# Kernel tuning notes

Hardware: AMD Instinct MI355X
Metric: run time of the kernel (lower is better)

The kernel has to match this reference:

```python
import jax, jax.numpy as jnp
import numpy as np

B, N, C = 2, 2048, 2048
H, KV = 16, 4          # query heads, kv heads
D = C // H             # head_dim = 128
ROPE_BASE = 10000.0


def rope_cos_sin(position_ids, dim):
    # interleaved RoPE: freqs for even indices, repeated pairwise to full dim
    inv_freq = 1.0 / (ROPE_BASE ** (jnp.arange(0, dim, 2, dtype=jnp.float32) / dim))
    ang = position_ids[..., None].astype(jnp.float32) * inv_freq   # [B, N, D/2]
    cos = jnp.repeat(jnp.cos(ang), 2, axis=-1)                     # [B, N, D]
    sin = jnp.repeat(jnp.sin(ang), 2, axis=-1)
    return cos, sin


def rotate_half_interleaved(x):
    # (x0, x1, x2, x3, ...) -> (-x1, x0, -x3, x2, ...)
    x1 = x[..., 0::2]
    x2 = x[..., 1::2]
    return jnp.stack([-x2, x1], axis=-1).reshape(x.shape)


def apply_rotary(x, cos, sin):
    # x: [B, h, N, D]; cos/sin: [B, N, D]
    return x * cos[:, None] + rotate_half_interleaved(x) * sin[:, None]


def setup_inputs() -> dict:
    key = jax.random.key(0)
    ks = jax.random.split(key, 5)
    s = 0.02
    return dict(
        x=jax.random.normal(ks[0], (B, N, C), jnp.float32),
        position_ids=jnp.tile(jnp.arange(N, dtype=jnp.int32), (B, 1)),
        Wq=jax.random.normal(ks[1], (C, C), jnp.float32) * s,
        bq=jnp.zeros((C,), jnp.float32),
        Wk=jax.random.normal(ks[2], (C, KV * D), jnp.float32) * s,
        bk=jnp.zeros((KV * D,), jnp.float32),
        Wv=jax.random.normal(ks[3], (C, KV * D), jnp.float32) * s,
        bv=jnp.zeros((KV * D,), jnp.float32),
        Wo=jax.random.normal(ks[4], (C, C), jnp.float32) * s,
    )


def reference(x, position_ids, Wq, bq, Wk, bk, Wv, bv, Wo):
    Bx, Nx, Cx = x.shape
    q = (x @ Wq + bq).reshape(Bx, Nx, H, D).transpose(0, 2, 1, 3)   # [B,H,N,D]
    k = (x @ Wk + bk).reshape(Bx, Nx, KV, D).transpose(0, 2, 1, 3)  # [B,KV,N,D]
    v = (x @ Wv + bv).reshape(Bx, Nx, KV, D).transpose(0, 2, 1, 3)

    cos, sin = rope_cos_sin(position_ids, D)
    q = apply_rotary(q, cos, sin)
    k = apply_rotary(k, cos, sin)

    # GQA expand: head h uses kv head h // groups (matches unsqueeze+expand+reshape)
    groups = H // KV
    k = jnp.repeat(k, groups, axis=1)   # [B,H,N,D]
    v = jnp.repeat(v, groups, axis=1)

    attn = jnp.einsum('bhqd,bhkd->bhqk', q, k) * (D ** -0.5)        # [B,H,N,N]
    causal_mask = jnp.triu(jnp.ones((Nx, Nx), dtype=bool), 1)
    attn = jnp.where(causal_mask, -jnp.inf, attn)
    attn = jax.nn.softmax(attn, axis=-1)

    out = jnp.einsum('bhqk,bhkd->bhqd', attn, v)
    out = out.transpose(0, 2, 1, 3).reshape(Bx, Nx, Cx)
    return out @ Wo
```

## Files before the change

kernel.cpp:

```cpp
#include <hip/hip_runtime.h>
#include <cstdint>
#include <type_traits>

typedef unsigned short u16;
typedef unsigned int u32;
typedef __bf16 bf16x8 __attribute__((ext_vector_type(8)));
typedef float f32x4 __attribute__((ext_vector_type(4)));

constexpr int BB = 2;
constexpr int SEQ = 2048;
constexpr int CH = 2048;
constexpr int NH = 16;
constexpr int NKV = 4;
constexpr int HD = 128;
constexpr int QKVC = CH + 2 * NKV * HD;

#define DI __device__ __forceinline__

DI u16 f2b(float x) {
  u32 u = __float_as_uint(x);
  u = u + 0x7FFFu + ((u >> 16) & 1u);
  return (u16)(u >> 16);
}
DI float b2f(u16 u) { return __uint_as_float(((u32)u) << 16); }

DI u32 pack2bf(float lo, float hi) {
  return __builtin_amdgcn_perm(__float_as_uint(hi), __float_as_uint(lo), 0x07060302u);
}

DI void glds16(const void* g, void* l) {
  __builtin_amdgcn_global_load_lds(
      (__attribute__((address_space(1))) void*)(uintptr_t)g,
      (__attribute__((address_space(3))) void*)(u32)(uintptr_t)l, 16, 0, 0);
}

__global__ __launch_bounds__(256) void xconv_kernel(const float* __restrict__ in,
                                                    u16* __restrict__ out, int n4) {
  int i = blockIdx.x * 256 + threadIdx.x;
  if (i < n4) {
    float4 v = *(const float4*)&in[(size_t)i * 4];
    ushort4 o;
    o.x = f2b(v.x); o.y = f2b(v.y); o.z = f2b(v.z); o.w = f2b(v.w);
    *(ushort4*)&out[(size_t)i * 4] = o;
  }
}

__global__ __launch_bounds__(256) void wtrans4_kernel(
    const float* __restrict__ Wq, const float* __restrict__ Wk,
    const float* __restrict__ Wv, const float* __restrict__ Wo,
    u16* __restrict__ wqkvt, u16* __restrict__ wot) {
  const int z = blockIdx.z;
  const float* in;
  u16* out;
  int Cc;
  if (z == 0)      { in = Wq; out = wqkvt;                                Cc = CH; }
  else if (z == 1) { in = Wk; out = wqkvt + (size_t)CH * CH;              Cc = NKV * HD; }
  else if (z == 2) { in = Wv; out = wqkvt + (size_t)(CH + NKV * HD) * CH; Cc = NKV * HD; }
  else             { in = Wo; out = wot;                                  Cc = CH; }
  if ((int)blockIdx.y * 64 >= Cc) return;

  __shared__ u16 tile[64 * 65];
  const int r0 = blockIdx.x * 64, c0 = blockIdx.y * 64;
  const int tid = threadIdx.x;
  for (int c = tid; c < 1024; c += 256) {
    int r = c >> 4, col = (c & 15) * 4;
    float4 v = *(const float4*)&in[(size_t)(r0 + r) * Cc + c0 + col];
    tile[r * 65 + col + 0] = f2b(v.x);
    tile[r * 65 + col + 1] = f2b(v.y);
    tile[r * 65 + col + 2] = f2b(v.z);
    tile[r * 65 + col + 3] = f2b(v.w);
  }
  __syncthreads();
  for (int c = tid; c < 1024; c += 256) {
    int r = c >> 4, col = (c & 15) * 4;
    ushort4 v;
    v.x = tile[(col + 0) * 65 + r];
    v.y = tile[(col + 1) * 65 + r];
    v.z = tile[(col + 2) * 65 + r];
    v.w = tile[(col + 3) * 65 + r];
    *(ushort4*)&out[(size_t)(c0 + r) * CH + r0 + col] = v;
  }
}

__global__ __launch_bounds__(256) void vtrans_kernel(const u16* __restrict__ in,
                                                     u16* __restrict__ out) {
  __shared__ u16 tile[64 * 65];
  const int s = blockIdx.z, n0 = blockIdx.x * 64, d0 = blockIdx.y * 64;
  const int tid = threadIdx.x;
  const u16* ip = in + (size_t)s * SEQ * HD + (size_t)n0 * HD + d0;
  u16* op = out + (size_t)s * HD * SEQ + (size_t)d0 * SEQ + n0;
  for (int c = tid; c < 1024; c += 256) {
    int r = c >> 4, col = (c & 15) * 4;
    ushort4 v = *(const ushort4*)&ip[(size_t)r * HD + col];
    tile[r * 65 + col + 0] = v.x;
    tile[r * 65 + col + 1] = v.y;
    tile[r * 65 + col + 2] = v.z;
    tile[r * 65 + col + 3] = v.w;
  }
  __syncthreads();
  for (int c = tid; c < 1024; c += 256) {
    int r = c >> 4, col = (c & 15) * 4;
    ushort4 v;
    v.x = tile[(col + 0) * 65 + r];
    v.y = tile[(col + 1) * 65 + r];
    v.z = tile[(col + 2) * 65 + r];
    v.w = tile[(col + 3) * 65 + r];
    int u = col;
    int w = (u & 3) | (((u >> 5) & 1) << 2) | (((u >> 2) & 3) << 3) | (((u >> 4) & 1) << 5);
    int glp = (w >> 3) ^ (r & 7);
    int colp = glp * 8 + (w & 7);
    *(ushort4*)&op[(size_t)r * SEQ + colp] = v;
  }
}

template <int MODE>
__global__ __launch_bounds__(512, 2) void gemm256_kernel(
    const u16* __restrict__ A, const u16* __restrict__ Bt,
    u16* __restrict__ Cb, float* __restrict__ Cf, u16* __restrict__ Vn,
    const float* __restrict__ bq, const float* __restrict__ bk,
    const float* __restrict__ bv, int M, int Nn, int K) {
  constexpr int BM = (MODE == 0) ? 256 : 128;
  constexpr int MI = BM / 32;
  constexpr int NPH = MI / 2;
  extern __shared__ char smem[];
  u16* As = (u16*)smem;
  u16* Bs = As + 2 * BM * 64;

  const int tid = threadIdx.x;
  const int lane = tid & 63, wave = tid >> 6;
  const int wrow = wave >> 2, wcol = wave & 3;
  const int lm = lane & 15, lq = lane >> 4;
  const int m0 = blockIdx.x * BM, n0 = blockIdx.y * 256;
  const int srow = tid >> 3;
  const int sswz = (tid & 7) ^ (srow & 7);

  f32x4 acc[MI][4] = {};

  auto stageA = [&](int kt, int b) {
#pragma unroll
    for (int s = 0; s < BM / 64; s++)
      glds16(A + (size_t)(m0 + s * 64 + srow) * K + kt + sswz * 8,
             (char*)As + b * (BM * 128) + (s * 64 + wave * 8) * 128);
  };
  auto stageB = [&](int kt, int b) {
#pragma unroll
    for (int s = 0; s < 4; s++)
      glds16(Bt + (size_t)(n0 + s * 64 + srow) * K + kt + sswz * 8,
             (char*)Bs + b * (256 * 128) + (s * 64 + wave * 8) * 128);
  };

  const int NT = K >> 6;
  stageA(0, 0);
  stageB(0, 0);
  asm volatile("s_waitcnt vmcnt(0)" ::: "memory");
  __builtin_amdgcn_s_barrier();

  for (int T = 0; T < NT; T++) {
    const int buf = T & 1;
    const u16* Asb = As + buf * (BM * 64);
    const u16* Bsb = Bs + buf * (256 * 64);
    const int kt1 = (T + 1) << 6;
    const bool pf = (T + 1 < NT);
    bf16x8 bfv[4][2];
#pragma unroll
    for (int q = 0; q < NPH; q++) {
      bf16x8 af[2][2];
#pragma unroll
      for (int ii = 0; ii < 2; ii++)
#pragma unroll
        for (int kk = 0; kk < 2; kk++)
          af[ii][kk] = *(const bf16x8*)&Asb[(wrow * (BM / 2) + (q * 2 + ii) * 16 + lm) * 64 +
                                            (((kk * 4 + lq) ^ (lm & 7)) * 8)];
      if (q == 0) {
#pragma unroll
        for (int j = 0; j < 4; j++)
#pragma unroll
          for (int kk = 0; kk < 2; kk++)
            bfv[j][kk] = *(const bf16x8*)&Bsb[(wcol * 64 + j * 16 + lm) * 64 +
                                              (((kk * 4 + lq) ^ (lm & 7)) * 8)];
        if (pf) {
          stageA(kt1, buf ^ 1);
          if (NPH == 2) stageB(kt1, buf ^ 1);
        }
      }
      if (NPH == 4 && q == 1 && pf) stageB(kt1, buf ^ 1);
      __builtin_amdgcn_s_barrier();
      asm volatile("s_waitcnt lgkmcnt(0)" ::: "memory");
      __builtin_amdgcn_sched_barrier(0);
      __builtin_amdgcn_s_setprio(1);
#pragma unroll
      for (int ii = 0; ii < 2; ii++)
#pragma unroll
        for (int j = 0; j < 4; j++)
#pragma unroll
          for (int kk = 0; kk < 2; kk++)
            acc[q * 2 + ii][j] = __builtin_amdgcn_mfma_f32_16x16x32_bf16(
                af[ii][kk], bfv[j][kk], acc[q * 2 + ii][j], 0, 0, 0);
      __builtin_amdgcn_s_setprio(0);
      if (q == NPH - 1) asm volatile("s_waitcnt vmcnt(0)" ::: "memory");
      __builtin_amdgcn_s_barrier();
    }
  }

#pragma unroll
  for (int i = 0; i < MI; i++) {
    const int mg = m0 + wrow * (BM / 2) + i * 16 + lq * 4;
#pragma unroll
    for (int j = 0; j < 4; j++) {
      const int ng = n0 + wcol * 64 + j * 16 + lm;
      float bias = 0.f;
      if (MODE == 0)
        bias = (ng < CH) ? bq[ng] : (ng < CH + NKV * HD ? bk[ng - CH] : bv[ng - CH - NKV * HD]);
#pragma unroll
      for (int r = 0; r < 4; r++) {
        float v = acc[i][j][r] + bias;
        if (MODE == 0) {
          if (ng >= CH + NKV * HD) {
            int tok = mg + r;
            int bidx = tok >> 11, n = tok & (SEQ - 1);
            int vcol = ng - (CH + NKV * HD);
            int kh = vcol >> 7, d = vcol & (HD - 1);
            Vn[((size_t)(bidx * NKV + kh) * SEQ + n) * HD + d] = f2b(v);
          } else {
            Cb[(size_t)(mg + r) * Nn + ng] = f2b(v);
          }
        } else {
          Cf[(size_t)(mg + r) * Nn + ng] = v;
        }
      }
    }
  }
}

__global__ __launch_bounds__(256) void rope_kernel(
    const u16* __restrict__ qkv, const int* __restrict__ pos,
    u16* __restrict__ Qo, u16* __restrict__ Ko) {
  __shared__ float cs_s[64], sn_s[64];
  const int tok = blockIdx.x;
  const int b = tok >> 11, n = tok & (SEQ - 1);
  const int t = threadIdx.x;
  const u16* row = qkv + (size_t)tok * QKVC;
  const float LN1E4_64 = 0.14391156831212788f;

  if (t < 64) {
    float ang = (float)pos[tok] * expf(-(float)t * LN1E4_64);
    float sn, cs;
    sincosf(ang, &sn, &cs);
    cs_s[t] = cs;
    sn_s[t] = sn;
  }
  __syncthreads();

  for (int idx = t; idx < NH * 64; idx += 256) {
    int hh = idx >> 6, i = idx & 63;
    float cs = cs_s[i], sn = sn_s[i];
    float q0v = b2f(row[hh * 128 + 2 * i]);
    float q1v = b2f(row[hh * 128 + 2 * i + 1]);
    size_t off = ((size_t)(b * NH + hh) * SEQ + n) * HD + 2 * i;
    Qo[off] = f2b(q0v * cs - q1v * sn);
    Qo[off + 1] = f2b(q1v * cs + q0v * sn);
  }
  {
    int kh = t >> 6, i = t & 63;
    float cs = cs_s[i], sn = sn_s[i];
    float k0v = b2f(row[CH + kh * 128 + 2 * i]);
    float k1v = b2f(row[CH + kh * 128 + 2 * i + 1]);
    int d0 = 2 * i;
    int g = d0 >> 3;
    int gp = (g & 8) | ((g ^ n) & 7);
    int dp = gp * 8 + (d0 & 7);
    size_t off = ((size_t)(b * NKV + kh) * SEQ + n) * HD + dp;
    Ko[off] = f2b(k0v * cs - k1v * sn);
    Ko[off + 1] = f2b(k1v * cs + k0v * sn);
  }
}

__global__ __launch_bounds__(256, 2) void flash_kernel(
    const u16* __restrict__ Q, const u16* __restrict__ Kk,
    const u16* __restrict__ Vt, u16* __restrict__ Oo) {
  __shared__ u16 Kb[2][64 * 128];
  __shared__ u16 Vb[2][144 * 64];
  const int tid = threadIdx.x, lane = tid & 63, wave = tid >> 6;
  const int lm = lane & 15, lq = lane >> 4;
  const int p = blockIdx.x;
  const int h = blockIdx.y, b = blockIdx.z;
  const int q0A = p * 64, q0B = (31 - p) * 64;
  const int kvh = h >> 2;
  const u16* Qg = Q + (size_t)(b * NH + h) * SEQ * HD;
  const u16* Kg = Kk + (size_t)(b * NKV + kvh) * SEQ * HD;
  const u16* Vg = Vt + (size_t)(b * NKV + kvh) * HD * SEQ;

  if (tid < 128) Vb[tid >> 6][128 * 64 + (tid & 63)] = 0x3F80;

  bf16x8 qf[2][4];
#pragma unroll
  for (int qg = 0; qg < 2; qg++) {
    const int q0g = qg ? q0B : q0A;
    const u16* qrow = Qg + (size_t)(q0g + wave * 16 + lm) * HD;
#pragma unroll
    for (int kd = 0; kd < 4; kd++)
      qf[qg][kd] = *(const bf16x8*)&qrow[kd * 32 + lq * 8];
  }

  f32x4 oacc[2][8] = {};
  f32x4 oaccS[2] = {};
  const float SCL2 = 0.12754325f;
  const int nIter = 32 - p;

  auto stage = [&](int kv0, int bufi) {
    const char* kb = (const char*)(Kg + (size_t)kv0 * HD);
    char* kl = (char*)&Kb[bufi][0];
    const char* vbb = (const char*)(Vg + (size_t)kv0);
    char* vl = (char*)&Vb[bufi][0];
#pragma unroll
    for (int c = 0; c < 4; c++) {
      int ch = wave * 4 + c;
      glds16(kb + ch * 1024 + lane * 16, kl + ch * 1024);
      glds16(vbb + (size_t)(ch * 8 + (lane >> 3)) * (SEQ * 2) + (lane & 7) * 16,
             vl + ch * 1024);
    }
  };

  stage(0, 0);

  for (int t = 0; t < nIter; t++) {
    __syncthreads();
    if (t + 1 < nIter) stage((t + 1) * 64, (t + 1) & 1);
    const u16* Ks = &Kb[t & 1][0];
    const u16* Vs = &Vb[t & 1][0];
    const int kv0 = t * 64;
    const bool actA = (t <= p);

    auto run = [&](auto dualc) {
      constexpr bool DUAL = decltype(dualc)::value;
      f32x4 sv[2][4] = {};
#pragma unroll
      for (int nt = 0; nt < 4; nt++)
#pragma unroll
        for (int kd = 0; kd < 4; kd++) {
          int g = kd * 4 + lq;
          int gpp = (g & 8) | ((g ^ lm) & 7);
          bf16x8 kf = *(const bf16x8*)&Ks[(nt * 16 + lm) * 128 + gpp * 8];
          sv[1][nt] = __builtin_amdgcn_mfma_f32_16x16x32_bf16(kf, qf[1][kd], sv[1][nt], 0, 0, 0);
          if constexpr (DUAL)
            sv[0][nt] = __builtin_amdgcn_mfma_f32_16x16x32_bf16(kf, qf[0][kd], sv[0][nt], 0, 0, 0);
        }

      alignas(16) u32 pad[2][2][4];
      auto softmax = [&](int qg, int q0g) {
        const int base = q0g + wave * 16;
        if (kv0 + 63 > base) {
          const int qrow = base + lm;
#pragma unroll
          for (int nt = 0; nt < 4; nt++) {
            float pv[4];
#pragma unroll
            for (int r = 0; r < 4; r++) {
              int kvg = kv0 + nt * 16 + lq * 4 + r;
              float e = exp2f(sv[qg][nt][r] * SCL2);
              pv[r] = (kvg > qrow) ? 0.f : e;
            }
            pad[qg][nt & 1][(nt >> 1) * 2 + 0] = pack2bf(pv[0], pv[1]);
            pad[qg][nt & 1][(nt >> 1) * 2 + 1] = pack2bf(pv[2], pv[3]);
          }
        } else {
#pragma unroll
          for (int nt = 0; nt < 4; nt++) {
            float pv[4];
#pragma unroll
            for (int r = 0; r < 4; r++) pv[r] = exp2f(sv[qg][nt][r] * SCL2);
            pad[qg][nt & 1][(nt >> 1) * 2 + 0] = pack2bf(pv[0], pv[1]);
            pad[qg][nt & 1][(nt >> 1) * 2 + 1] = pack2bf(pv[2], pv[3]);
          }
        }
      };
      softmax(1, q0B);
      if constexpr (DUAL) softmax(0, q0A);

#pragma unroll
      for (int ks = 0; ks < 2; ks++) {
        const int glp = (ks * 4 + lq) ^ (lm & 7);
        const bf16x8 pa1 = *(const bf16x8*)&pad[1][ks][0];
        const bf16x8 pa0 = *(const bf16x8*)&pad[0][ks][0];
#pragma unroll
        for (int dt = 0; dt < 8; dt++) {
          bf16x8 vf = *(const bf16x8*)&Vs[(dt * 16 + lm) * 64 + glp * 8];
          oacc[1][dt] = __builtin_amdgcn_mfma_f32_16x16x32_bf16(pa1, vf, oacc[1][dt], 0, 0, 0);
          if constexpr (DUAL)
            oacc[0][dt] = __builtin_amdgcn_mfma_f32_16x16x32_bf16(pa0, vf, oacc[0][dt], 0, 0, 0);
        }
        bf16x8 vf8 = *(const bf16x8*)&Vs[(128 + lm) * 64 + glp * 8];
        oaccS[1] = __builtin_amdgcn_mfma_f32_16x16x32_bf16(pa1, vf8, oaccS[1], 0, 0, 0);
        if constexpr (DUAL)
          oaccS[0] = __builtin_amdgcn_mfma_f32_16x16x32_bf16(pa0, vf8, oaccS[0], 0, 0, 0);
      }
    };
    if (actA) run(std::integral_constant<bool, true>{});
    else      run(std::integral_constant<bool, false>{});
  }

  u16* orow = Oo + (size_t)b * SEQ * CH + (size_t)h * HD;
#pragma unroll
  for (int qg = 0; qg < 2; qg++) {
    const int q0g = qg ? q0B : q0A;
    float inv[4];
#pragma unroll
    for (int r = 0; r < 4; r++) inv[r] = 1.0f / __shfl(oaccS[qg][r], lq * 16);
    const int qrow_base = q0g + wave * 16 + lq * 4;
#pragma unroll
    for (int dt = 0; dt < 8; dt++)
#pragma unroll
      for (int r = 0; r < 4; r++)
        orow[(size_t)(qrow_base + r) * CH + dt * 16 + lm] = f2b(oacc[qg][dt][r] * inv[r]);
  }
}

extern "C" void kernel_launch(void* const* d_in, const int* in_sizes, int n_in,
                              void* d_out, int out_size, void* d_ws, size_t ws_size,
                              hipStream_t stream) {
  const float* x = (const float*)d_in[0];
  const int* pos = (const int*)d_in[1];
  const float* Wq = (const float*)d_in[2];
  const float* bq = (const float*)d_in[3];
  const float* Wk = (const float*)d_in[4];
  const float* bk = (const float*)d_in[5];
  const float* Wv = (const float*)d_in[6];
  const float* bv = (const float*)d_in[7];
  const float* Wo = (const float*)d_in[8];
  float* out = (float*)d_out;

  char* ws = (char*)d_ws;
  u16* xb = (u16*)ws;    ws += (size_t)BB * SEQ * CH * 2;
  u16* wqkvt = (u16*)ws; ws += (size_t)QKVC * CH * 2;
  u16* wot = (u16*)ws;   ws += (size_t)CH * CH * 2;
  u16* qkv = (u16*)ws;   ws += (size_t)BB * SEQ * QKVC * 2;
  u16* qr = (u16*)ws;    ws += (size_t)BB * NH * SEQ * HD * 2;
  u16* kr = (u16*)ws;    ws += (size_t)BB * NKV * SEQ * HD * 2;
  u16* vn = (u16*)ws;    ws += (size_t)BB * NKV * SEQ * HD * 2;
  u16* vt = (u16*)ws;    ws += (size_t)BB * NKV * SEQ * HD * 2;
  u16* ao = (u16*)ws;    ws += (size_t)BB * SEQ * CH * 2;

  static int attr_done = 0;
  if (!attr_done) {
    hipFuncSetAttribute(reinterpret_cast<const void*>(gemm256_kernel<0>),
                        hipFuncAttributeMaxDynamicSharedMemorySize, 131072);
    hipFuncSetAttribute(reinterpret_cast<const void*>(gemm256_kernel<1>),
                        hipFuncAttributeMaxDynamicSharedMemorySize, 131072);
    attr_done = 1;
  }

  xconv_kernel<<<dim3(BB * SEQ * CH / 1024), 256, 0, stream>>>(x, xb, BB * SEQ * CH / 4);
  wtrans4_kernel<<<dim3(32, 32, 4), 256, 0, stream>>>(Wq, Wk, Wv, Wo, wqkvt, wot);
  gemm256_kernel<0><<<dim3(16, 12), 512, 131072, stream>>>(xb, wqkvt, qkv, (float*)nullptr,
                                                           vn, bq, bk, bv, BB * SEQ, QKVC, CH);
  rope_kernel<<<dim3(BB * SEQ), 256, 0, stream>>>(qkv, pos, qr, kr);
  vtrans_kernel<<<dim3(SEQ / 64, HD / 64, BB * NKV), 256, 0, stream>>>(vn, vt);
  flash_kernel<<<dim3(16, NH, BB), 256, 0, stream>>>(qr, kr, vt, ao);
  gemm256_kernel<1><<<dim3(32, 8), 512, 98304, stream>>>(ao, wot, (u16*)nullptr, out, nullptr,
                                                         nullptr, nullptr, nullptr, BB * SEQ, CH, CH);
}
```

Before: 305.2 us.

## Restructure GEMM main loop into quadrant phases with split staging and partial vmcnt waits

Reworks the 256-wide GEMM's inner loop. For the QKV mode, each K-step is split into four M/N quadrant phases that reload A and B fragments per quadrant. Global-to-LDS staging of the next tile is split into halves interleaved across those phases, and waits use partial vmcnt counts instead of draining every load at the end of the step. The aim is to overlap global loads with MFMA work more finely and to reduce register pressure from holding all B fragments at once. The hand-tuned vmcnt counts and the new per-wave row mapping are fragile, and a wrong count could race on LDS.

```diff
diff --git a/kernel.cpp b/kernel.cpp
--- a/kernel.cpp
+++ b/kernel.cpp
@@ -121,7 +121,6 @@
     const float* __restrict__ bv, int M, int Nn, int K) {
   constexpr int BM = (MODE == 0) ? 256 : 128;
   constexpr int MI = BM / 32;
-  constexpr int NPH = MI / 2;
   extern __shared__ char smem[];
   u16* As = (u16*)smem;
   u16* Bs = As + 2 * BM * 64;
@@ -131,74 +130,148 @@
   const int wrow = wave >> 2, wcol = wave & 3;
   const int lm = lane & 15, lq = lane >> 4;
   const int m0 = blockIdx.x * BM, n0 = blockIdx.y * 256;
-  const int srow = tid >> 3;
-  const int sswz = (tid & 7) ^ (srow & 7);
+  const int l8 = lane >> 3;
+  const int sswz8 = ((lane & 7) ^ l8) * 8;
 
   f32x4 acc[MI][4] = {};
 
-  auto stageA = [&](int kt, int b) {
-#pragma unroll
-    for (int s = 0; s < BM / 64; s++)
-      glds16(A + (size_t)(m0 + s * 64 + srow) * K + kt + sswz * 8,
-             (char*)As + b * (BM * 128) + (s * 64 + wave * 8) * 128);
+  auto stageA = [&](int kt, int bsel, int half) {
+    if constexpr (MODE == 0) {
+#pragma unroll
+      for (int j = 0; j < 2; j++) {
+        const int rb = wave * 8 + j * 128 + half * 64;
+        glds16(A + (size_t)(m0 + rb + l8) * K + kt + sswz8,
+               (char*)As + bsel * (BM * 128) + rb * 128);
+      }
+    } else {
+      const int rb = (wave & 3) * 8 + (wave >> 2) * 64 + half * 32;
+      glds16(A + (size_t)(m0 + rb + l8) * K + kt + sswz8,
+             (char*)As + bsel * (BM * 128) + rb * 128);
+    }
   };
-  auto stageB = [&](int kt, int b) {
-#pragma unroll
-    for (int s = 0; s < 4; s++)
-      glds16(Bt + (size_t)(n0 + s * 64 + srow) * K + kt + sswz * 8,
-             (char*)Bs + b * (256 * 128) + (s * 64 + wave * 8) * 128);
+  auto stageB = [&](int kt, int bsel, int half) {
+#pragma unroll
+    for (int j = 0; j < 2; j++) {
+      const int rb = (wave & 3) * 8 + (j * 2 + (wave >> 2)) * 64 + half * 32;
+      glds16(Bt + (size_t)(n0 + rb + l8) * K + kt + sswz8,
+             (char*)Bs + bsel * 32768 + rb * 128);
+    }
   };
 
   const int NT = K >> 6;
-  stageA(0, 0);
-  stageB(0, 0);
+  stageA(0, 0, 0); stageB(0, 0, 0); stageB(0, 0, 1); stageA(0, 0, 1);
   asm volatile("s_waitcnt vmcnt(0)" ::: "memory");
   __builtin_amdgcn_s_barrier();
 
-  for (int T = 0; T < NT; T++) {
-    const int buf = T & 1;
-    const u16* Asb = As + buf * (BM * 64);
-    const u16* Bsb = Bs + buf * (256 * 64);
-    const int kt1 = (T + 1) << 6;
-    const bool pf = (T + 1 < NT);
-    bf16x8 bfv[4][2];
-#pragma unroll
-    for (int q = 0; q < NPH; q++) {
+  if constexpr (MODE == 0) {
+    bf16x8 bf[2][2][2];
+    for (int T = 0; T < NT; T++) {
+      const int buf = T & 1;
+      const u16* Asb = As + buf * (BM * 64);
+      const u16* Bsb = Bs + buf * (256 * 64);
+      const int kt1 = (T + 1) << 6;
+      const bool pf = (T + 1 < NT);
+      bf16x8 af[4][2];
+#pragma unroll
+      for (int q = 0; q < 4; q++) {
+        const int qm = q >> 1, qn = q & 1;
+        if (qn == 0) {
+#pragma unroll
+          for (int ii = 0; ii < 4; ii++)
+#pragma unroll
+            for (int kk = 0; kk < 2; kk++)
+              af[ii][kk] = *(const bf16x8*)&Asb[(wrow * 128 + qm * 64 + ii * 16 + lm) * 64 +
+                                                ((kk * 4 + lq) ^ (lm & 7)) * 8];
+        }
+        if (q < 2) {
+#pragma unroll
+          for (int jj = 0; jj < 2; jj++)
+#pragma unroll
+            for (int kk = 0; kk < 2; kk++)
+              bf[qn][jj][kk] = *(const bf16x8*)&Bsb[(wcol * 64 + qn * 32 + jj * 16 + lm) * 64 +
+                                                    ((kk * 4 + lq) ^ (lm & 7)) * 8];
+        }
+        if (pf) {
+          if (q == 0) stageA(kt1, buf ^ 1, 0);
+          else if (q == 1) stageB(kt1, buf ^ 1, 0);
+          else if (q == 2) stageB(kt1, buf ^ 1, 1);
+          else stageA(kt1, buf ^ 1, 1);
+        }
+        __builtin_amdgcn_s_barrier();
+        asm volatile("s_waitcnt lgkmcnt(0)" ::: "memory");
+        __builtin_amdgcn_sched_barrier(0);
+        __builtin_amdgcn_s_setprio(1);
+#pragma unroll
+        for (int kk = 0; kk < 2; kk++)
+#pragma unroll
+          for (int ii = 0; ii < 4; ii++)
+#pragma unroll
+            for (int jj = 0; jj < 2; jj++)
+              acc[qm * 4 + ii][qn * 2 + jj] = __builtin_amdgcn_mfma_f32_16x16x32_bf16(
+                  af[ii][kk], bf[qn][jj][kk], acc[qm * 4 + ii][qn * 2 + jj], 0, 0, 0);
+        __builtin_amdgcn_s_setprio(0);
+        if (q == 0) {
+          if (pf) asm volatile("s_waitcnt vmcnt(4)" ::: "memory");
+          else    asm volatile("s_waitcnt vmcnt(2)" ::: "memory");
+        } else if (q == 1) {
+          if (pf) asm volatile("s_waitcnt vmcnt(4)" ::: "memory");
+          else    asm volatile("s_waitcnt vmcnt(0)" ::: "memory");
+        } else if (q == 3 && pf) {
+          asm volatile("s_waitcnt vmcnt(4)" ::: "memory");
+        }
+        __builtin_amdgcn_s_barrier();
+      }
+    }
+  } else {
+    bf16x8 bf1[4][2];
+    for (int T = 0; T < NT; T++) {
+      const int buf = T & 1;
+      const u16* Asb = As + buf * (BM * 64);
+      const u16* Bsb = Bs + buf * (256 * 64);
+      const int kt1 = (T + 1) << 6;
+      const bool pf = (T + 1 < NT);
       bf16x8 af[2][2];
 #pragma unroll
-      for (int ii = 0; ii < 2; ii++)
+      for (int q = 0; q < 2; q++) {
+#pragma unroll
+        for (int ii = 0; ii < 2; ii++)
+#pragma unroll
+          for (int kk = 0; kk < 2; kk++)
+            af[ii][kk] = *(const bf16x8*)&Asb[(wrow * 64 + (q * 2 + ii) * 16 + lm) * 64 +
+                                              ((kk * 4 + lq) ^ (lm & 7)) * 8];
+        if (q == 0) {
+#pragma unroll
+          for (int j = 0; j < 4; j++)
+#pragma unroll
+            for (int kk = 0; kk < 2; kk++)
+              bf1[j][kk] = *(const bf16x8*)&Bsb[(wcol * 64 + j * 16 + lm) * 64 +
+                                                ((kk * 4 + lq) ^ (lm & 7)) * 8];
+        }
+        if (pf) {
+          if (q == 0) { stageA(kt1, buf ^ 1, 0); stageB(kt1, buf ^ 1, 0); stageB(kt1, buf ^ 1, 1); }
+          else stageA(kt1, buf ^ 1, 1);
+        }
+        __builtin_amdgcn_s_barrier();
+        asm volatile("s_waitcnt lgkmcnt(0)" ::: "memory");
+        __builtin_amdgcn_sched_barrier(0);
+        __builtin_amdgcn_s_setprio(1);
 #pragma unroll
         for (int kk = 0; kk < 2; kk++)
-          af[ii][kk] = *(const bf16x8*)&Asb[(wrow * (BM / 2) + (q * 2 + ii) * 16 + lm) * 64 +
-                                            (((kk * 4 + lq) ^ (lm & 7)) * 8)];
-      if (q == 0) {
-#pragma unroll
-        for (int j = 0; j < 4; j++)
-#pragma unroll
-          for (int kk = 0; kk < 2; kk++)
-            bfv[j][kk] = *(const bf16x8*)&Bsb[(wcol * 64 + j * 16 + lm) * 64 +
-                                              (((kk * 4 + lq) ^ (lm & 7)) * 8)];
-        if (pf) {
-          stageA(kt1, buf ^ 1);
-          if (NPH == 2) stageB(kt1, buf ^ 1);
-        }
+#pragma unroll
+          for (int ii = 0; ii < 2; ii++)
+#pragma unroll
+            for (int j = 0; j < 4; j++)
+              acc[q * 2 + ii][j] = __builtin_amdgcn_mfma_f32_16x16x32_bf16(
+                  af[ii][kk], bf1[j][kk], acc[q * 2 + ii][j], 0, 0, 0);
+        __builtin_amdgcn_s_setprio(0);
+        if (q == 0) {
+          if (pf) asm volatile("s_waitcnt vmcnt(5)" ::: "memory");
+          else    asm volatile("s_waitcnt vmcnt(0)" ::: "memory");
+        } else if (pf) {
+          asm volatile("s_waitcnt vmcnt(1)" ::: "memory");
+        }
+        __builtin_amdgcn_s_barrier();
       }
-      if (NPH == 4 && q == 1 && pf) stageB(kt1, buf ^ 1);
-      __builtin_amdgcn_s_barrier();
-      asm volatile("s_waitcnt lgkmcnt(0)" ::: "memory");
-      __builtin_amdgcn_sched_barrier(0);
-      __builtin_amdgcn_s_setprio(1);
-#pragma unroll
-      for (int ii = 0; ii < 2; ii++)
-#pragma unroll
-        for (int j = 0; j < 4; j++)
-#pragma unroll
-          for (int kk = 0; kk < 2; kk++)
-            acc[q * 2 + ii][j] = __builtin_amdgcn_mfma_f32_16x16x32_bf16(
-                af[ii][kk], bfv[j][kk], acc[q * 2 + ii][j], 0, 0, 0);
-      __builtin_amdgcn_s_setprio(0);
-      if (q == NPH - 1) asm volatile("s_waitcnt vmcnt(0)" ::: "memory");
-      __builtin_amdgcn_s_barrier();
     }
   }
 
```

Measured after the change: 314.1 us. +2.9%, slower.
